# Kernel optimization log

Measured on AMD Instinct MI355X. Metric: run time of the kernel, lower is better.

The kernel has to match this reference:

```python
import jax, jax.numpy as jnp
import numpy as np

N = 100000
E = 800000
IN_NF, IN_EF, OUT_NF, H1, H2 = 64, 16, 64, 32, 32

def _mlp(x, ws, bs):
    last = len(ws) - 1
    for i, (W, b) in enumerate(zip(ws, bs)):
        x = x @ W + b
        if i < last:
            x = jax.nn.leaky_relu(x, 0.2)
    return x

def setup_inputs():
    key = jax.random.key(0)
    ks = iter(jax.random.split(key, 80))
    inp = {}
    inp["nf"] = jax.random.normal(next(ks), (N, IN_NF), jnp.float32)
    inp["ef_out"] = jax.random.normal(next(ks), (E, IN_EF), jnp.float32)
    inp["ef_in"] = jax.random.normal(next(ks), (E, IN_EF), jnp.float32)
    def add_mlp(prefix, sizes):
        for i in range(1, len(sizes)):
            lim = 1.0 / np.sqrt(sizes[i - 1])
            inp[prefix + "_w" + str(i - 1)] = jax.random.uniform(next(ks), (sizes[i - 1], sizes[i]), jnp.float32, -lim, lim)
            inp[prefix + "_b" + str(i - 1)] = jax.random.uniform(next(ks), (sizes[i],), jnp.float32, -lim, lim)
    add_mlp("o2i", (2 * IN_NF + IN_EF, 64, 64, 64, 64, 2 * OUT_NF))
    add_mlp("i2o", (2 * IN_NF + IN_EF, 64, 64, 64, 1 + H1 + H2))
    add_mlp("ri", (IN_NF + 2 * OUT_NF, 64, 64, 64, OUT_NF))
    add_mlp("ro", (IN_NF + H1 + H2, 64, 64, 64, OUT_NF))
    inp["src_out"] = jax.random.randint(next(ks), (E,), 0, N)
    inp["dst_out"] = jax.random.randint(next(ks), (E,), 0, N)
    inp["src_in"] = jax.random.randint(next(ks), (E,), 0, N)
    inp["dst_in"] = jax.random.randint(next(ks), (E,), 0, N)
    idx = jnp.arange(N)
    inp["input_mask"] = idx < (2 * N) // 5
    inp["output_mask"] = idx >= (3 * N) // 5
    return inp

def _forward(nf, ef_out, ef_in, o2i_ws, o2i_bs, i2o_ws, i2o_bs, ri_ws, ri_bs, ro_ws, ro_bs,
             src_out, dst_out, src_in, dst_in, input_mask, output_mask):
    # net_out etype: gather src/dst node feats + edge feats -> MLP -> sum scatter to dst
    xi = jnp.concatenate([nf[src_out], nf[dst_out], ef_out], axis=1)  # [E, 2*in_nf+in_ef]
    efi = _mlp(xi, o2i_ws, o2i_bs)                                    # [E, 2*out_nf]
    nfi = jax.ops.segment_sum(efi, dst_out, num_segments=N)
    new_i = _mlp(jnp.concatenate([nf, nfi], axis=1), ri_ws, ri_bs)    # [N, out_nf]
    # net_in etype: gated edge messages -> mean / max scatter to dst
    xo = jnp.concatenate([nf[src_in], nf[dst_in], ef_in], axis=1)
    m = _mlp(xo, i2o_ws, i2o_bs)                                      # [E, 1+h1+h2]
    k = jax.nn.sigmoid(m[:, :1])
    f1 = m[:, 1:1 + H1] * k
    f2 = m[:, 1 + H1:] * k
    cnt = jax.ops.segment_sum(jnp.ones((E,), nf.dtype), dst_in, num_segments=N)
    nfo1 = jax.ops.segment_sum(f1, dst_in, num_segments=N) / jnp.maximum(cnt, 1.0)[:, None]
    mx = jax.ops.segment_max(f2, dst_in, num_segments=N)
    nfo2 = jnp.where(cnt[:, None] > 0, mx, 0.0)                       # DGL max gives 0 on empty
    new_o = _mlp(jnp.concatenate([nf, nfo1, nfo2], axis=1), ro_ws, ro_bs)
    out = jnp.where(input_mask[:, None], new_i, 0.0)
    out = jnp.where(output_mask[:, None], new_o, out)
    return out

def reference(nf, ef_out, ef_in,
              o2i_w0, o2i_b0, o2i_w1, o2i_b1, o2i_w2, o2i_b2, o2i_w3, o2i_b3, o2i_w4, o2i_b4,
              i2o_w0, i2o_b0, i2o_w1, i2o_b1, i2o_w2, i2o_b2, i2o_w3, i2o_b3,
              ri_w0, ri_b0, ri_w1, ri_b1, ri_w2, ri_b2, ri_w3, ri_b3,
              ro_w0, ro_b0, ro_w1, ro_b1, ro_w2, ro_b2, ro_w3, ro_b3,
              src_out, dst_out, src_in, dst_in, input_mask, output_mask):
    return _forward(nf, ef_out, ef_in,
                    [o2i_w0, o2i_w1, o2i_w2, o2i_w3, o2i_w4], [o2i_b0, o2i_b1, o2i_b2, o2i_b3, o2i_b4],
                    [i2o_w0, i2o_w1, i2o_w2, i2o_w3], [i2o_b0, i2o_b1, i2o_b2, i2o_b3],
                    [ri_w0, ri_w1, ri_w2, ri_w3], [ri_b0, ri_b1, ri_b2, ri_b3],
                    [ro_w0, ro_w1, ro_w2, ro_w3], [ro_b0, ro_b1, ro_b2, ro_b3],
                    src_out, dst_out, src_in, dst_in, input_mask, output_mask)
```

## Files before the change

### kernel.cpp

```cpp
#include <hip/hip_runtime.h>
#include <cmath>

#define THREADS 256

static constexpr int N_NODES   = 100000;
static constexpr int N_EDGES   = 800000;
static constexpr int NIN       = 40000;
static constexpr int NOUT_BASE = 60000;
static constexpr int NOUT      = 40000;
static constexpr int LIST_CAP  = 400000;
static constexpr int CBLK      = 1024;
static constexpr int NBLK      = (N_EDGES + CBLK - 1) / CBLK;

static constexpr size_t OFF_NFI   = 0;
static constexpr size_t OFF_F1    = OFF_NFI   + (size_t)NIN  * 64;
static constexpr size_t OFF_F2    = OFF_F1    + (size_t)NOUT * 32;
static constexpr size_t OFF_CNT   = OFF_F2    + (size_t)NOUT * 32;
static constexpr size_t OFF_CNTO  = OFF_CNT   + NOUT;
static constexpr size_t OFF_CTRO  = OFF_CNTO  + NIN;
static constexpr size_t OFF_CTRI  = OFF_CTRO  + 1;
static constexpr size_t OFF_ZEND  = OFF_CTRI  + 1;
static constexpr size_t OFF_BVEC  = OFF_ZEND;
static constexpr size_t OFF_BCO   = OFF_BVEC + 64;
static constexpr size_t OFF_BCI   = OFF_BCO + NBLK;
static constexpr size_t OFF_LISTO = (OFF_BCI + NBLK + 1) & ~(size_t)1;
static constexpr size_t OFF_LISTI = OFF_LISTO + 2 * (size_t)LIST_CAP;
static constexpr size_t OFF_WB    = (OFF_LISTI + 2 * (size_t)LIST_CAP + 3) & ~(size_t)3;
static constexpr size_t OFF_NFB   = OFF_WB + 47936;

static constexpr unsigned OW_O2I0  = 0;
static constexpr unsigned OW_O2I1  = 10752;
static constexpr unsigned OW_O2I2  = 15360;
static constexpr unsigned OW_O2I3  = 19968;
static constexpr unsigned OW_O2I4C = 24576;
static constexpr unsigned OW_I2O0  = 29184;
static constexpr unsigned OW_I2O1  = 39936;
static constexpr unsigned OW_I2O2  = 44544;
static constexpr unsigned OW_I2O3  = 49152;
static constexpr unsigned OW_RI0   = 54912;
static constexpr unsigned OW_RI1   = 59520;
static constexpr unsigned OW_RI2   = 64128;
static constexpr unsigned OW_RI3   = 68736;
static constexpr unsigned OW_RO0   = 73344;
static constexpr unsigned OW_RO1   = 82048;
static constexpr unsigned OW_RO2   = 86656;
static constexpr unsigned OW_RO3   = 91264;

typedef __attribute__((ext_vector_type(8))) short short8;
typedef __attribute__((ext_vector_type(4))) float f32x4;

__device__ __forceinline__ float lrelu(float x) { return x > 0.0f ? x : 0.2f * x; }

__device__ __forceinline__ unsigned short f2b(float f) {
    unsigned u = __float_as_uint(f);
    return (unsigned short)((u + 0x7fffu + ((u >> 16) & 1u)) >> 16);
}
__device__ __forceinline__ unsigned pk2(float a, float b) {
    return (unsigned)f2b(a) | ((unsigned)f2b(b) << 16);
}
__device__ __forceinline__ short8 cvt8(const float4 va, const float4 vb) {
    union { uint4 u; short8 s; } t;
    t.u = make_uint4(pk2(va.x, va.y), pk2(va.z, va.w), pk2(vb.x, vb.y), pk2(vb.z, vb.w));
    return t.s;
}
__device__ __forceinline__ unsigned fkey(float f) {
    unsigned u = __float_as_uint(f);
    return (u & 0x80000000u) ? ~u : (u | 0x80000000u);
}
__device__ __forceinline__ float funkey(unsigned k) {
    return (k & 0x80000000u) ? __uint_as_float(k & 0x7fffffffu) : __uint_as_float(~k);
}
__device__ __forceinline__ uint2 packm(unsigned s, int d, int e) {
    return make_uint2(s | ((unsigned)(d & 0x7FFF) << 17),
                      (unsigned)e | (((unsigned)d >> 15) << 20));
}

template<int MT, int NT, int KT, int XSTR, int WSTR>
__device__ __forceinline__ void gemm_core(const unsigned short* X, const unsigned short* W,
                                          const float* bias, int biasN, int wv, int lane,
                                          f32x4 (&acc)[MT][NT]) {
    const int r = lane & 15, kg = lane >> 4;
    short8 a[MT][KT];
#pragma unroll
    for (int mt = 0; mt < MT; ++mt)
#pragma unroll
        for (int kk = 0; kk < KT; ++kk)
            a[mt][kk] = *(const short8*)(X + (wv * 16 * MT + mt * 16 + r) * XSTR + kk * 32 + kg * 8);
#pragma unroll
    for (int nt = 0; nt < NT; ++nt) {
        const int c = nt * 16 + r;
        const float bv = (c < biasN) ? bias[c] : 0.0f;
#pragma unroll
        for (int mt = 0; mt < MT; ++mt) acc[mt][nt] = (f32x4){bv, bv, bv, bv};
    }
#pragma unroll
    for (int kk = 0; kk < KT; ++kk)
#pragma unroll
        for (int nt = 0; nt < NT; ++nt) {
            short8 b = *(const short8*)(W + (nt * 16 + r) * WSTR + kk * 32 + kg * 8);
#pragma unroll
            for (int mt = 0; mt < MT; ++mt)
                acc[mt][nt] = __builtin_amdgcn_mfma_f32_16x16x32_bf16(a[mt][kk], b, acc[mt][nt], 0, 0, 0);
        }
}

template<int MT, int NT, int XSTR>
__device__ __forceinline__ void writeback(unsigned short* X, f32x4 (&acc)[MT][NT], int wv, int lane) {
    const int r = lane & 15, kg = lane >> 4;
#pragma unroll
    for (int mt = 0; mt < MT; ++mt)
#pragma unroll
        for (int nt = 0; nt < NT; ++nt)
#pragma unroll
            for (int q = 0; q < 4; ++q)
                X[(wv * 16 * MT + mt * 16 + kg * 4 + q) * XSTR + nt * 16 + r] = f2b(lrelu(acc[mt][nt][q]));
}

template<int NT, int KT, int XSTR, int WSTR>
__device__ __forceinline__ void gemm_w1(const unsigned short* Xw, const unsigned short* W,
                                        const float* bv, int lane, f32x4 (&acc)[NT]) {
    const int r = lane & 15, kg = lane >> 4;
    short8 a[KT];
#pragma unroll
    for (int kk = 0; kk < KT; ++kk)
        a[kk] = *(const short8*)(Xw + r * XSTR + kk * 32 + kg * 8);
#pragma unroll
    for (int nt = 0; nt < NT; ++nt) acc[nt] = (f32x4){bv[nt], bv[nt], bv[nt], bv[nt]};
#pragma unroll
    for (int kk = 0; kk < KT; ++kk)
#pragma unroll
        for (int nt = 0; nt < NT; ++nt) {
            short8 b = *(const short8*)(W + (nt * 16 + r) * WSTR + kk * 32 + kg * 8);
            acc[nt] = __builtin_amdgcn_mfma_f32_16x16x32_bf16(a[kk], b, acc[nt], 0, 0, 0);
        }
}

template<int NT, int XSTR>
__device__ __forceinline__ void writeback_w1(unsigned short* Xw, f32x4 (&acc)[NT], int lane) {
    const int r = lane & 15, kg = lane >> 4;
#pragma unroll
    for (int nt = 0; nt < NT; ++nt)
#pragma unroll
        for (int q = 0; q < 4; ++q)
            Xw[(kg * 4 + q) * XSTR + nt * 16 + r] = f2b(lrelu(acc[nt][q]));
}

struct WDesc { const float* w; int K, N, stride, Np; unsigned off; };
struct WTab { WDesc d[16]; };

__global__ __launch_bounds__(THREADS)
void convert_w(WTab t, unsigned short* wts) {
    const WDesc d = t.d[blockIdx.y];
    const int idx = blockIdx.x * THREADS + threadIdx.x;
    const int tot = d.Np * d.stride;
    if (idx >= tot) return;
    const int n = idx / d.stride, k = idx - n * d.stride;
    const float v = (k < d.K && n < d.N) ? d.w[(size_t)k * d.N + n] : 0.0f;
    wts[d.off + idx] = f2b(v);
}

__global__ __launch_bounds__(THREADS)
void compose_k(const float* __restrict__ w4, const float* __restrict__ rw0,
               const float* __restrict__ b4, unsigned short* __restrict__ wts,
               float* __restrict__ bvec) {
    const int idx = blockIdx.x * THREADS + threadIdx.x;
    if (idx < 4096) {
        const int n = idx >> 6, k = idx & 63;
        float s = 0.0f;
        for (int j = 0; j < 128; ++j) s += w4[k * 128 + j] * rw0[(size_t)(64 + j) * 64 + n];
        wts[OW_O2I4C + n * 72 + k] = f2b(s);
    } else if (idx < 4160) {
        const int n = idx - 4096;
        float s = 0.0f;
        for (int j = 0; j < 128; ++j) s += b4[j] * rw0[(size_t)(64 + j) * 64 + n];
        bvec[n] = s;
    }
}

__global__ __launch_bounds__(THREADS)
void conv_nf_k(const float* __restrict__ nf, unsigned short* __restrict__ nfb) {
    const int i = blockIdx.x * THREADS + threadIdx.x;
    if (i >= N_NODES * 8) return;
    const float4 va = ((const float4*)nf)[i * 2], vb = ((const float4*)nf)[i * 2 + 1];
    *(uint4*)(nfb + (size_t)i * 8) =
        make_uint4(pk2(va.x, va.y), pk2(va.z, va.w), pk2(vb.x, vb.y), pk2(vb.z, vb.w));
}

__global__ __launch_bounds__(THREADS)
void count_k(const int* __restrict__ dst_out, const int* __restrict__ dst_in,
             unsigned* __restrict__ bco, unsigned* __restrict__ bci,
             unsigned* __restrict__ cnt, unsigned* __restrict__ cnto) {
    const int base = blockIdx.x * CBLK;
    const int tid = threadIdx.x, lane = tid & 63, wv = tid >> 6;
    __shared__ unsigned so[4], si[4];
    unsigned co = 0, ci = 0;
#pragma unroll
    for (int it = 0; it < CBLK / THREADS; ++it) {
        const int e = base + it * THREADS + tid;
        bool po = false, pi = false;
        if (e < N_EDGES) {
            const int d0 = dst_out[e];
            if (d0 < NIN) { po = true; atomicAdd(cnto + d0, 1u); }
            const int d1 = dst_in[e];
            if (d1 >= NOUT_BASE) { pi = true; atomicAdd(cnt + (d1 - NOUT_BASE), 1u); }
        }
        const unsigned long long mo = __ballot(po), mi = __ballot(pi);
        if (lane == 0) { co += (unsigned)__popcll(mo); ci += (unsigned)__popcll(mi); }
    }
    if (lane == 0) { so[wv] = co; si[wv] = ci; }
    __syncthreads();
    if (tid == 0) {
        bco[blockIdx.x] = so[0] + so[1] + so[2] + so[3];
        bci[blockIdx.x] = si[0] + si[1] + si[2] + si[3];
    }
}

__global__ __launch_bounds__(128)
void scan_k(unsigned* __restrict__ bco, unsigned* __restrict__ bci,
            unsigned* __restrict__ ctro, unsigned* __restrict__ ctri) {
    const int lane = threadIdx.x & 63;
    unsigned* arr = (threadIdx.x < 64) ? bco : bci;
    unsigned* tot = (threadIdx.x < 64) ? ctro : ctri;
    const int per = (NBLK + 63) / 64;
    const int lo = lane * per;
    const int hi = (lo + per < NBLK) ? lo + per : NBLK;
    unsigned s = 0;
    for (int i = lo; i < hi; ++i) s += arr[i];
    unsigned incl = s;
    for (int d = 1; d < 64; d <<= 1) {
        unsigned v = __shfl_up(incl, d);
        if (lane >= d) incl += v;
    }
    unsigned run = incl - s;
    for (int i = lo; i < hi; ++i) { const unsigned c = arr[i]; arr[i] = run; run += c; }
    if (lane == 63) *tot = incl;
}

__global__ __launch_bounds__(THREADS)
void emit_k(const int* __restrict__ src_out, const int* __restrict__ dst_out,
            const int* __restrict__ src_in, const int* __restrict__ dst_in,
            const unsigned* __restrict__ bco, const unsigned* __restrict__ bci,
            uint2* __restrict__ listo, uint2* __restrict__ listi) {
    const int base = blockIdx.x * CBLK;
    const int tid = threadIdx.x, lane = tid & 63;
    const unsigned long long lm = (1ull << lane) - 1ull;
    __shared__ unsigned lco, lci;
    if (tid == 0) { lco = bco[blockIdx.x]; lci = bci[blockIdx.x]; }
    __syncthreads();
#pragma unroll
    for (int it = 0; it < CBLK / THREADS; ++it) {
        const int e = base + it * THREADS + tid;
        bool po = false, pi = false;
        int d0 = 0, d1 = 0;
        if (e < N_EDGES) {
            d0 = dst_out[e]; po = d0 < NIN;
            d1 = dst_in[e];  pi = d1 >= NOUT_BASE;
        }
        const unsigned long long mo = __ballot(po), mi = __ballot(pi);
        unsigned b0v = 0, b1v = 0;
        if (lane == 0) {
            if (mo) b0v = atomicAdd(&lco, (unsigned)__popcll(mo));
            if (mi) b1v = atomicAdd(&lci, (unsigned)__popcll(mi));
        }
        b0v = (unsigned)__shfl((int)b0v, 0);
        b1v = (unsigned)__shfl((int)b1v, 0);
        if (po) listo[b0v + (unsigned)__popcll(mo & lm)] = packm((unsigned)src_out[e], d0, e);
        if (pi) listi[b1v + (unsigned)__popcll(mi & lm)] = packm((unsigned)src_in[e], d1, e);
    }
}

__device__ __forceinline__ void gather_a(short8 (&a)[5], const unsigned short* nfb, const float* ef,
                                         int e16, int s16, int d16, int kg) {
    const short8 z = {0, 0, 0, 0, 0, 0, 0, 0};
    if (e16 >= 0) {
        const unsigned short* ps = nfb + (size_t)s16 * 64 + kg * 8;
        const unsigned short* pd = nfb + (size_t)d16 * 64 + kg * 8;
        a[0] = *(const short8*)ps;
        a[1] = *(const short8*)(ps + 32);
        a[2] = *(const short8*)pd;
        a[3] = *(const short8*)(pd + 32);
        if (kg < 2) {
            const float* pe = ef + (size_t)e16 * 16 + kg * 8;
            a[4] = cvt8(((const float4*)pe)[0], ((const float4*)pe)[1]);
        } else a[4] = z;
    } else { a[0] = z; a[1] = z; a[2] = z; a[3] = z; a[4] = z; }
}

__global__ __launch_bounds__(512, 4)
void edge_out_mfma(const unsigned short* __restrict__ nfb, const float* __restrict__ ef,
                   const uint2* __restrict__ list, const unsigned* __restrict__ counter,
                   const unsigned short* __restrict__ wts,
                   const float* __restrict__ b0, const float* __restrict__ b1,
                   const float* __restrict__ b2, const float* __restrict__ b3,
                   float* __restrict__ nfi) {
    __shared__ unsigned short W[24576];
    __shared__ unsigned short X[128 * 72];
    const int tid = threadIdx.x, lane = tid & 63, wv = tid >> 6;
    const int r = lane & 15, kg = lane >> 4;
    for (int i = tid * 8; i < 24576; i += 512 * 8)
        *(uint4*)(W + i) = *(const uint4*)(wts + OW_O2I0 + i);
    float bv0[4], bv1[4], bv2[4], bv3[4];
    const float bz[4] = {0.0f, 0.0f, 0.0f, 0.0f};
#pragma unroll
    for (int nt = 0; nt < 4; ++nt) {
        bv0[nt] = b0[nt * 16 + r]; bv1[nt] = b1[nt * 16 + r];
        bv2[nt] = b2[nt * 16 + r]; bv3[nt] = b3[nt * 16 + r];
    }
    unsigned short* Xw = X + wv * 16 * 72;
    const unsigned short* W4C = wts + OW_O2I4C;
    const unsigned total = *counter;
    const unsigned nchunks = (total + 15) >> 4;
    __syncthreads();

    for (unsigned c = blockIdx.x * 8 + wv; c < nchunks; c += (unsigned)gridDim.x * 8) {
        const unsigned ebase = c << 4;
        int my_e = -1, my_s = 0, my_d = -1;
        if (lane < 16 && ebase + (unsigned)lane < total) {
            const uint2 m = list[ebase + lane];
            my_s = (int)(m.x & 0x1FFFFu);
            my_d = (int)(((m.x >> 17) & 0x7FFFu) | (((m.y >> 20) & 3u) << 15));
            my_e = (int)(m.y & 0xFFFFFu);
        }
        const int e16 = __shfl(my_e, r), s16 = __shfl(my_s, r), d16 = __shfl(my_d, r);
        short8 a[5];
        gather_a(a, nfb, ef, e16, s16, d16, kg);
        f32x4 acc[4];
#pragma unroll
        for (int nt = 0; nt < 4; ++nt) acc[nt] = (f32x4){bv0[nt], bv0[nt], bv0[nt], bv0[nt]};
#pragma unroll
        for (int kk = 0; kk < 5; ++kk)
#pragma unroll
            for (int nt = 0; nt < 4; ++nt) {
                short8 b = *(const short8*)(W + (nt * 16 + r) * 168 + kk * 32 + kg * 8);
                acc[nt] = __builtin_amdgcn_mfma_f32_16x16x32_bf16(a[kk], b, acc[nt], 0, 0, 0);
            }
        writeback_w1<4, 72>(Xw, acc, lane);
        gemm_w1<4, 2, 72, 72>(Xw, W + 10752, bv1, lane, acc); writeback_w1<4, 72>(Xw, acc, lane);
        gemm_w1<4, 2, 72, 72>(Xw, W + 15360, bv2, lane, acc); writeback_w1<4, 72>(Xw, acc, lane);
        gemm_w1<4, 2, 72, 72>(Xw, W + 19968, bv3, lane, acc); writeback_w1<4, 72>(Xw, acc, lane);
        f32x4 acc4[4];
        gemm_w1<4, 2, 72, 72>(Xw, W4C, bz, lane, acc4);
        int re[4], rd[4];
#pragma unroll
        for (int q = 0; q < 4; ++q) {
            re[q] = __shfl(my_e, kg * 4 + q);
            rd[q] = __shfl(my_d, kg * 4 + q);
        }
        float s[4];
        int cur = -1;
#pragma unroll
        for (int q = 0; q < 4; ++q) {
            if (re[q] < 0) break;
            if (rd[q] != cur) {
                if (cur >= 0) {
                    float* p = nfi + (size_t)cur * 64;
#pragma unroll
                    for (int nt = 0; nt < 4; ++nt) atomicAdd(p + nt * 16 + r, s[nt]);
                }
                cur = rd[q];
#pragma unroll
                for (int nt = 0; nt < 4; ++nt) s[nt] = acc4[nt][q];
            } else {
#pragma unroll
                for (int nt = 0; nt < 4; ++nt) s[nt] += acc4[nt][q];
            }
        }
        if (cur >= 0) {
            float* p = nfi + (size_t)cur * 64;
#pragma unroll
            for (int nt = 0; nt < 4; ++nt) atomicAdd(p + nt * 16 + r, s[nt]);
        }
    }
}

__global__ __launch_bounds__(512, 4)
void edge_in_mfma(const unsigned short* __restrict__ nfb, const float* __restrict__ ef,
                  const uint2* __restrict__ list, const unsigned* __restrict__ counter,
                  const unsigned short* __restrict__ wts,
                  const float* __restrict__ b0, const float* __restrict__ b1,
                  const float* __restrict__ b2, const float* __restrict__ b3,
                  float* __restrict__ f1s, unsigned* __restrict__ f2k) {
    __shared__ unsigned short W[25728];
    __shared__ unsigned short X[128 * 72];
    const int tid = threadIdx.x, lane = tid & 63, wv = tid >> 6;
    const int r = lane & 15, kg = lane >> 4;
    for (int i = tid * 8; i < 25728; i += 512 * 8)
        *(uint4*)(W + i) = *(const uint4*)(wts + OW_I2O0 + i);
    float bv0[4], bv1[4], bv2[4], bv3[5];
#pragma unroll
    for (int nt = 0; nt < 4; ++nt) {
        bv0[nt] = b0[nt * 16 + r]; bv1[nt] = b1[nt * 16 + r]; bv2[nt] = b2[nt * 16 + r];
        bv3[nt] = b3[nt * 16 + r];
    }
    bv3[4] = (r == 0) ? b3[64] : 0.0f;
    unsigned short* Xw = X + wv * 16 * 72;
    const unsigned total = *counter;
    const unsigned nchunks = (total + 15) >> 4;
    bool valid[5], isadd[5];
#pragma unroll
    for (int nt = 0; nt < 5; ++nt) {
        const int cc = nt * 16 + r;
        valid[nt] = (cc >= 1 && cc <= 64);
        isadd[nt] = (cc <= 32);
    }
    __syncthreads();

    for (unsigned c = blockIdx.x * 8 + wv; c < nchunks; c += (unsigned)gridDim.x * 8) {
        const unsigned ebase = c << 4;
        int my_e = -1, my_s = 0, my_d = -1;
        if (lane < 16 && ebase + (unsigned)lane < total) {
            const uint2 m = list[ebase + lane];
            my_s = (int)(m.x & 0x1FFFFu);
            my_d = (int)(((m.x >> 17) & 0x7FFFu) | (((m.y >> 20) & 3u) << 15));
            my_e = (int)(m.y & 0xFFFFFu);
        }
        const int e16 = __shfl(my_e, r), s16 = __shfl(my_s, r), d16 = __shfl(my_d, r);
        short8 a[5];
        gather_a(a, nfb, ef, e16, s16, d16, kg);
        f32x4 acc[4];
#pragma unroll
        for (int nt = 0; nt < 4; ++nt) acc[nt] = (f32x4){bv0[nt], bv0[nt], bv0[nt], bv0[nt]};
#pragma unroll
        for (int kk = 0; kk < 5; ++kk)
#pragma unroll
            for (int nt = 0; nt < 4; ++nt) {
                short8 b = *(const short8*)(W + (nt * 16 + r) * 168 + kk * 32 + kg * 8);
                acc[nt] = __builtin_amdgcn_mfma_f32_16x16x32_bf16(a[kk], b, acc[nt], 0, 0, 0);
            }
        writeback_w1<4, 72>(Xw, acc, lane);
        gemm_w1<4, 2, 72, 72>(Xw, W + 10752, bv1, lane, acc); writeback_w1<4, 72>(Xw, acc, lane);
        gemm_w1<4, 2, 72, 72>(Xw, W + 15360, bv2, lane, acc); writeback_w1<4, 72>(Xw, acc, lane);
        f32x4 acc5[5];
        gemm_w1<5, 2, 72, 72>(Xw, W + 19968, bv3, lane, acc5);
        int re[4], rd[4];
        float rgv[4];
#pragma unroll
        for (int q = 0; q < 4; ++q) {
            re[q]  = __shfl(my_e, kg * 4 + q);
            rd[q]  = __shfl(my_d, kg * 4 + q);
            rgv[q] = __shfl(acc5[4][q], lane & 48);
        }
        float s[5];
        int cur = -1;
        auto flush = [&](int d) {
            if (d < 0) return;
            const int rr = d - NOUT_BASE;
            if (valid[0]) atomicAdd(f1s + (size_t)rr * 32 + (r - 1), s[0]);
            if (valid[1]) atomicAdd(f1s + (size_t)rr * 32 + 15 + r, s[1]);
            if (valid[2]) {
                if (isadd[2]) atomicAdd(f1s + (size_t)rr * 32 + 31, s[2]);
                else          atomicMax(f2k + (size_t)rr * 32 + (r - 1), fkey(s[2]));
            }
            if (valid[3]) atomicMax(f2k + (size_t)rr * 32 + 15 + r, fkey(s[3]));
            if (valid[4]) atomicMax(f2k + (size_t)rr * 32 + 31, fkey(s[4]));
        };
#pragma unroll
        for (int q = 0; q < 4; ++q) {
            if (re[q] < 0) break;
            const float kgv = 1.0f / (1.0f + expf(-rgv[q]));
            if (rd[q] != cur) {
                flush(cur);
                cur = rd[q];
#pragma unroll
                for (int nt = 0; nt < 5; ++nt) s[nt] = acc5[nt][q] * kgv;
            } else {
#pragma unroll
                for (int nt = 0; nt < 5; ++nt) {
                    const float v = acc5[nt][q] * kgv;
                    s[nt] = isadd[nt] ? s[nt] + v : fmaxf(s[nt], v);
                }
            }
        }
        flush(cur);
    }
}

__global__ __launch_bounds__(THREADS)
void node_ri_mfma(const unsigned short* __restrict__ nfb, const float* __restrict__ nfi,
                  const unsigned* __restrict__ cnto, const float* __restrict__ bvec,
                  const unsigned short* __restrict__ wts,
                  const float* __restrict__ b0, const float* __restrict__ b1,
                  const float* __restrict__ b2, const float* __restrict__ b3,
                  float* __restrict__ out) {
    __shared__ unsigned short X[64 * 72];
    __shared__ unsigned short Wl[4608];
    const int tid = threadIdx.x, lane = tid & 63, wv = tid >> 6;
    const int base = blockIdx.x * 64;
    for (int i = tid; i < 64 * 8; i += THREADS) {
        const int el = i >> 3, q = i & 7;
        *(uint4*)(X + el * 72 + q * 8) = *(const uint4*)(nfb + (size_t)(base + el) * 64 + q * 8);
    }
    auto stage = [&](unsigned off) {
        for (int i = tid * 8; i < 4608; i += THREADS * 8)
            *(uint4*)(Wl + i) = *(const uint4*)(wts + off + i);
    };
    stage(OW_RI0);
    __syncthreads();
    const int r = lane & 15, kg = lane >> 4;
    f32x4 acc[1][4];
    gemm_core<1, 4, 2, 72, 72>(X, Wl, b0, 64, wv, lane, acc);
    {
        float bvv[4];
#pragma unroll
        for (int nt = 0; nt < 4; ++nt) bvv[nt] = bvec[nt * 16 + r];
#pragma unroll
        for (int q = 0; q < 4; ++q) {
            const int node = base + wv * 16 + kg * 4 + q;
            const float cf = (float)cnto[node];
#pragma unroll
            for (int nt = 0; nt < 4; ++nt)
                acc[0][nt][q] += nfi[(size_t)node * 64 + nt * 16 + r] + cf * bvv[nt];
        }
    }
    writeback<1, 4, 72>(X, acc, wv, lane);
    __syncthreads(); stage(OW_RI1); __syncthreads();
    gemm_core<1, 4, 2, 72, 72>(X, Wl, b1, 64, wv, lane, acc);
    writeback<1, 4, 72>(X, acc, wv, lane);
    __syncthreads(); stage(OW_RI2); __syncthreads();
    gemm_core<1, 4, 2, 72, 72>(X, Wl, b2, 64, wv, lane, acc);
    writeback<1, 4, 72>(X, acc, wv, lane);
    __syncthreads(); stage(OW_RI3); __syncthreads();
    gemm_core<1, 4, 2, 72, 72>(X, Wl, b3, 64, wv, lane, acc);
#pragma unroll
    for (int nt = 0; nt < 4; ++nt)
#pragma unroll
        for (int q = 0; q < 4; ++q)
            out[(size_t)(base + wv * 16 + kg * 4 + q) * 64 + nt * 16 + r] = acc[0][nt][q];
}

__global__ __launch_bounds__(THREADS)
void node_ro_mfma(const float* __restrict__ nf, const float* __restrict__ f1s,
                  const unsigned* __restrict__ f2k, const unsigned* __restrict__ cnt,
                  const unsigned short* __restrict__ wts,
                  const float* __restrict__ b0, const float* __restrict__ b1,
                  const float* __restrict__ b2, const float* __restrict__ b3,
                  float* __restrict__ out) {
    __shared__ unsigned short X[64 * 136];
    __shared__ unsigned short Wl[8704];
    const int tid = threadIdx.x, lane = tid & 63, wv = tid >> 6;
    const int rbase = blockIdx.x * 64;
    for (int i = tid; i < 64 * 17; i += THREADS) {
        const int el = i / 17, q = i - el * 17;
        const int rr = rbase + el;
        unsigned p0 = 0, p1 = 0, p2 = 0, p3 = 0;
        if (q < 16) {
            float v[8];
            if (q < 8) {
                const float* sp = nf + (size_t)(NOUT_BASE + rr) * 64 + q * 8;
                const float4 va = *(const float4*)sp, vb = *(const float4*)(sp + 4);
                v[0]=va.x; v[1]=va.y; v[2]=va.z; v[3]=va.w; v[4]=vb.x; v[5]=vb.y; v[6]=vb.z; v[7]=vb.w;
            } else {
                const unsigned cc = cnt[rr];
                if (q < 12) {
                    const float inv = 1.0f / fmaxf((float)cc, 1.0f);
#pragma unroll
                    for (int j = 0; j < 8; ++j) v[j] = f1s[(size_t)rr * 32 + (q - 8) * 8 + j] * inv;
                } else {
#pragma unroll
                    for (int j = 0; j < 8; ++j)
                        v[j] = (cc > 0u) ? funkey(f2k[(size_t)rr * 32 + (q - 12) * 8 + j]) : 0.0f;
                }
            }
            p0 = pk2(v[0], v[1]); p1 = pk2(v[2], v[3]); p2 = pk2(v[4], v[5]); p3 = pk2(v[6], v[7]);
        }
        *(uint4*)(X + el * 136 + q * 8) = make_uint4(p0, p1, p2, p3);
    }
    auto stage = [&](unsigned off, int n) {
        for (int i = tid * 8; i < n; i += THREADS * 8)
            *(uint4*)(Wl + i) = *(const uint4*)(wts + off + i);
    };
    stage(OW_RO0, 8704);
    __syncthreads();
    f32x4 acc[1][4];
    gemm_core<1, 4, 4, 136, 136>(X, Wl, b0, 64, wv, lane, acc);
    writeback<1, 4, 136>(X, acc, wv, lane);
    __syncthreads(); stage(OW_RO1, 4608); __syncthreads();
    gemm_core<1, 4, 2, 136, 72>(X, Wl, b1, 64, wv, lane, acc);
    writeback<1, 4, 136>(X, acc, wv, lane);
    __syncthreads(); stage(OW_RO2, 4608); __syncthreads();
    gemm_core<1, 4, 2, 136, 72>(X, Wl, b2, 64, wv, lane, acc);
    writeback<1, 4, 136>(X, acc, wv, lane);
    __syncthreads(); stage(OW_RO3, 4608); __syncthreads();
    gemm_core<1, 4, 2, 136, 72>(X, Wl, b3, 64, wv, lane, acc);
    const int r = lane & 15, kg = lane >> 4;
#pragma unroll
    for (int nt = 0; nt < 4; ++nt)
#pragma unroll
        for (int q = 0; q < 4; ++q)
            out[(size_t)(NOUT_BASE + rbase + wv * 16 + kg * 4 + q) * 64 + nt * 16 + r] = acc[0][nt][q];
}

extern "C" void kernel_launch(void* const* d_in, const int* in_sizes, int n_in,
                              void* d_out, int out_size, void* d_ws, size_t ws_size,
                              hipStream_t stream) {
    const float* nf     = (const float*)d_in[0];
    const float* ef_out = (const float*)d_in[1];
    const float* ef_in  = (const float*)d_in[2];
    const float* o2i_w[5] = {(const float*)d_in[3], (const float*)d_in[5], (const float*)d_in[7], (const float*)d_in[9], (const float*)d_in[11]};
    const float* o2i_b[5] = {(const float*)d_in[4], (const float*)d_in[6], (const float*)d_in[8], (const float*)d_in[10], (const float*)d_in[12]};
    const float* i2o_w[4] = {(const float*)d_in[13], (const float*)d_in[15], (const float*)d_in[17], (const float*)d_in[19]};
    const float* i2o_b[4] = {(const float*)d_in[14], (const float*)d_in[16], (const float*)d_in[18], (const float*)d_in[20]};
    const float* ri_w[4]  = {(const float*)d_in[21], (const float*)d_in[23], (const float*)d_in[25], (const float*)d_in[27]};
    const float* ri_b[4]  = {(const float*)d_in[22], (const float*)d_in[24], (const float*)d_in[26], (const float*)d_in[28]};
    const float* ro_w[4]  = {(const float*)d_in[29], (const float*)d_in[31], (const float*)d_in[33], (const float*)d_in[35]};
    const float* ro_b[4]  = {(const float*)d_in[30], (const float*)d_in[32], (const float*)d_in[34], (const float*)d_in[36]};
    const int* src_out  = (const int*)d_in[37];
    const int* dst_out  = (const int*)d_in[38];
    const int* src_in   = (const int*)d_in[39];
    const int* dst_in   = (const int*)d_in[40];

    unsigned* ws    = (unsigned*)d_ws;
    float*    nfi   = (float*)(ws + OFF_NFI);
    float*    f1s   = (float*)(ws + OFF_F1);
    unsigned* f2k   = ws + OFF_F2;
    unsigned* cnt   = ws + OFF_CNT;
    unsigned* cnto  = ws + OFF_CNTO;
    unsigned* ctro  = ws + OFF_CTRO;
    unsigned* ctri  = ws + OFF_CTRI;
    float*    bvec  = (float*)(ws + OFF_BVEC);
    unsigned* bco   = ws + OFF_BCO;
    unsigned* bci   = ws + OFF_BCI;
    uint2*    lsto  = (uint2*)(ws + OFF_LISTO);
    uint2*    lsti  = (uint2*)(ws + OFF_LISTI);
    unsigned short* wts = (unsigned short*)(ws + OFF_WB);
    unsigned short* nfb = (unsigned short*)(ws + OFF_NFB);

    hipMemsetAsync(d_ws, 0, OFF_ZEND * sizeof(unsigned), stream);
    hipMemsetAsync((char*)d_out + (size_t)NIN * 64 * sizeof(float), 0,
                   (size_t)(NOUT_BASE - NIN) * 64 * sizeof(float), stream);

    WTab t;
    t.d[0]  = {o2i_w[0], 144,  64, 168,  64, OW_O2I0};
    t.d[1]  = {o2i_w[1],  64,  64,  72,  64, OW_O2I1};
    t.d[2]  = {o2i_w[2],  64,  64,  72,  64, OW_O2I2};
    t.d[3]  = {o2i_w[3],  64,  64,  72,  64, OW_O2I3};
    t.d[4]  = {i2o_w[0], 144,  64, 168,  64, OW_I2O0};
    t.d[5]  = {i2o_w[1],  64,  64,  72,  64, OW_I2O1};
    t.d[6]  = {i2o_w[2],  64,  64,  72,  64, OW_I2O2};
    t.d[7]  = {i2o_w[3],  64,  65,  72,  80, OW_I2O3};
    t.d[8]  = {ri_w[0],   64,  64,  72,  64, OW_RI0};
    t.d[9]  = {ri_w[1],   64,  64,  72,  64, OW_RI1};
    t.d[10] = {ri_w[2],   64,  64,  72,  64, OW_RI2};
    t.d[11] = {ri_w[3],   64,  64,  72,  64, OW_RI3};
    t.d[12] = {ro_w[0],  128,  64, 136,  64, OW_RO0};
    t.d[13] = {ro_w[1],   64,  64,  72,  64, OW_RO1};
    t.d[14] = {ro_w[2],   64,  64,  72,  64, OW_RO2};
    t.d[15] = {ro_w[3],   64,  64,  72,  64, OW_RO3};
    convert_w<<<dim3(50, 16), THREADS, 0, stream>>>(t, wts);
    compose_k<<<17, THREADS, 0, stream>>>(o2i_w[4], ri_w[0], o2i_b[4], wts, bvec);
    conv_nf_k<<<(N_NODES * 8 + THREADS - 1) / THREADS, THREADS, 0, stream>>>(nf, nfb);

    count_k<<<NBLK, THREADS, 0, stream>>>(dst_out, dst_in, bco, bci, cnt, cnto);
    scan_k<<<1, 128, 0, stream>>>(bco, bci, ctro, ctri);
    emit_k<<<NBLK, THREADS, 0, stream>>>(src_out, dst_out, src_in, dst_in, bco, bci, lsto, lsti);

    edge_out_mfma<<<512, 512, 0, stream>>>(
        nfb, ef_out, lsto, ctro, wts,
        o2i_b[0], o2i_b[1], o2i_b[2], o2i_b[3], nfi);

    edge_in_mfma<<<512, 512, 0, stream>>>(
        nfb, ef_in, lsti, ctri, wts,
        i2o_b[0], i2o_b[1], i2o_b[2], i2o_b[3], f1s, f2k);

    node_ri_mfma<<<NIN / 64, THREADS, 0, stream>>>(
        nfb, nfi, cnto, bvec, wts, ri_b[0], ri_b[1], ri_b[2], ri_b[3], (float*)d_out);

    node_ro_mfma<<<NOUT / 64, THREADS, 0, stream>>>(
        nf, f1s, f2k, cnt, wts, ro_b[0], ro_b[1], ro_b[2], ro_b[3], (float*)d_out);
}
```

Measured before the change: 323.9 us.

## Replace compacted edge lists with destination-sorted counting-sort buckets

Swaps block-level stream compaction of filtered edges for a full counting sort by destination node. A histogram kernel is followed by a two-block exclusive scan over per-node counts, and emit then scatters each edge to its node's slot through per-node atomics. Edges sharing a destination end up contiguous, which is meant to improve locality and cut atomic contention in the downstream segment-sum, mean and max reductions inside the edge MFMA kernels. The cost is a scan over 40k nodes done by a single block per list and scattered atomic writes in emit. The ctr counters and bvec move out of the zeroed region, and ctr now comes from the scan.

```diff
diff --git a/kernel.cpp b/kernel.cpp
--- a/kernel.cpp
+++ b/kernel.cpp
@@ -9,21 +9,19 @@
 static constexpr int NOUT_BASE = 60000;
 static constexpr int NOUT      = 40000;
 static constexpr int LIST_CAP  = 400000;
-static constexpr int CBLK      = 1024;
-static constexpr int NBLK      = (N_EDGES + CBLK - 1) / CBLK;
 
 static constexpr size_t OFF_NFI   = 0;
 static constexpr size_t OFF_F1    = OFF_NFI   + (size_t)NIN  * 64;
 static constexpr size_t OFF_F2    = OFF_F1    + (size_t)NOUT * 32;
 static constexpr size_t OFF_CNT   = OFF_F2    + (size_t)NOUT * 32;
 static constexpr size_t OFF_CNTO  = OFF_CNT   + NOUT;
-static constexpr size_t OFF_CTRO  = OFF_CNTO  + NIN;
+static constexpr size_t OFF_ZEND  = OFF_CNTO  + NIN;
+static constexpr size_t OFF_CTRO  = OFF_ZEND;
 static constexpr size_t OFF_CTRI  = OFF_CTRO  + 1;
-static constexpr size_t OFF_ZEND  = OFF_CTRI  + 1;
-static constexpr size_t OFF_BVEC  = OFF_ZEND;
-static constexpr size_t OFF_BCO   = OFF_BVEC + 64;
-static constexpr size_t OFF_BCI   = OFF_BCO + NBLK;
-static constexpr size_t OFF_LISTO = (OFF_BCI + NBLK + 1) & ~(size_t)1;
+static constexpr size_t OFF_BVEC  = OFF_CTRI  + 1;
+static constexpr size_t OFF_OFFSO = OFF_BVEC + 64;
+static constexpr size_t OFF_OFFSI = OFF_OFFSO + NIN;
+static constexpr size_t OFF_LISTO = (OFF_OFFSI + NOUT + 1) & ~(size_t)1;
 static constexpr size_t OFF_LISTI = OFF_LISTO + 2 * (size_t)LIST_CAP;
 static constexpr size_t OFF_WB    = (OFF_LISTI + 2 * (size_t)LIST_CAP + 3) & ~(size_t)3;
 static constexpr size_t OFF_NFB   = OFF_WB + 47936;
@@ -187,85 +185,58 @@
 }
 
 __global__ __launch_bounds__(THREADS)
-void count_k(const int* __restrict__ dst_out, const int* __restrict__ dst_in,
-             unsigned* __restrict__ bco, unsigned* __restrict__ bci,
-             unsigned* __restrict__ cnt, unsigned* __restrict__ cnto) {
-    const int base = blockIdx.x * CBLK;
+void hist_k(const int* __restrict__ dst_out, const int* __restrict__ dst_in,
+            unsigned* __restrict__ cnto, unsigned* __restrict__ cnt) {
+    const int e = blockIdx.x * THREADS + threadIdx.x;
+    const int d0 = dst_out[e];
+    if (d0 < NIN) atomicAdd(cnto + d0, 1u);
+    const int d1 = dst_in[e];
+    if (d1 >= NOUT_BASE) atomicAdd(cnt + (d1 - NOUT_BASE), 1u);
+}
+
+__global__ __launch_bounds__(1024)
+void scan2_k(const unsigned* __restrict__ cnto, const unsigned* __restrict__ cnt,
+             unsigned* __restrict__ offso, unsigned* __restrict__ offsi,
+             unsigned* __restrict__ ctro, unsigned* __restrict__ ctri) {
+    const unsigned* h = (blockIdx.x == 0) ? cnto : cnt;
+    unsigned* o       = (blockIdx.x == 0) ? offso : offsi;
+    unsigned* tot     = (blockIdx.x == 0) ? ctro : ctri;
     const int tid = threadIdx.x, lane = tid & 63, wv = tid >> 6;
-    __shared__ unsigned so[4], si[4];
-    unsigned co = 0, ci = 0;
-#pragma unroll
-    for (int it = 0; it < CBLK / THREADS; ++it) {
-        const int e = base + it * THREADS + tid;
-        bool po = false, pi = false;
-        if (e < N_EDGES) {
-            const int d0 = dst_out[e];
-            if (d0 < NIN) { po = true; atomicAdd(cnto + d0, 1u); }
-            const int d1 = dst_in[e];
-            if (d1 >= NOUT_BASE) { pi = true; atomicAdd(cnt + (d1 - NOUT_BASE), 1u); }
-        }
-        const unsigned long long mo = __ballot(po), mi = __ballot(pi);
-        if (lane == 0) { co += (unsigned)__popcll(mo); ci += (unsigned)__popcll(mi); }
-    }
-    if (lane == 0) { so[wv] = co; si[wv] = ci; }
+    const int lo = tid * 40;
+    const int hi = (lo + 40 < NIN) ? lo + 40 : NIN;
+    unsigned s = 0;
+    for (int i = lo; i < hi; ++i) s += h[i];
+    unsigned incl = s;
+    for (int d = 1; d < 64; d <<= 1) { unsigned v = __shfl_up(incl, d); if (lane >= d) incl += v; }
+    __shared__ unsigned wsum[16], woff[16];
+    if (lane == 63) wsum[wv] = incl;
     __syncthreads();
-    if (tid == 0) {
-        bco[blockIdx.x] = so[0] + so[1] + so[2] + so[3];
-        bci[blockIdx.x] = si[0] + si[1] + si[2] + si[3];
-    }
-}
-
-__global__ __launch_bounds__(128)
-void scan_k(unsigned* __restrict__ bco, unsigned* __restrict__ bci,
-            unsigned* __restrict__ ctro, unsigned* __restrict__ ctri) {
-    const int lane = threadIdx.x & 63;
-    unsigned* arr = (threadIdx.x < 64) ? bco : bci;
-    unsigned* tot = (threadIdx.x < 64) ? ctro : ctri;
-    const int per = (NBLK + 63) / 64;
-    const int lo = lane * per;
-    const int hi = (lo + per < NBLK) ? lo + per : NBLK;
-    unsigned s = 0;
-    for (int i = lo; i < hi; ++i) s += arr[i];
-    unsigned incl = s;
-    for (int d = 1; d < 64; d <<= 1) {
-        unsigned v = __shfl_up(incl, d);
-        if (lane >= d) incl += v;
-    }
-    unsigned run = incl - s;
-    for (int i = lo; i < hi; ++i) { const unsigned c = arr[i]; arr[i] = run; run += c; }
-    if (lane == 63) *tot = incl;
+    if (tid < 16) {
+        unsigned v = wsum[tid], sc = v;
+        for (int d = 1; d < 16; d <<= 1) { unsigned t2 = __shfl_up(sc, d); if (tid >= d) sc += t2; }
+        woff[tid] = sc - v;
+    }
+    __syncthreads();
+    unsigned run = woff[wv] + incl - s;
+    for (int i = lo; i < hi; ++i) { const unsigned c = h[i]; o[i] = run; run += c; }
+    if (hi == NIN && lo < NIN) *tot = run;
 }
 
 __global__ __launch_bounds__(THREADS)
 void emit_k(const int* __restrict__ src_out, const int* __restrict__ dst_out,
             const int* __restrict__ src_in, const int* __restrict__ dst_in,
-            const unsigned* __restrict__ bco, const unsigned* __restrict__ bci,
+            unsigned* __restrict__ offso, unsigned* __restrict__ offsi,
             uint2* __restrict__ listo, uint2* __restrict__ listi) {
-    const int base = blockIdx.x * CBLK;
-    const int tid = threadIdx.x, lane = tid & 63;
-    const unsigned long long lm = (1ull << lane) - 1ull;
-    __shared__ unsigned lco, lci;
-    if (tid == 0) { lco = bco[blockIdx.x]; lci = bci[blockIdx.x]; }
-    __syncthreads();
-#pragma unroll
-    for (int it = 0; it < CBLK / THREADS; ++it) {
-        const int e = base + it * THREADS + tid;
-        bool po = false, pi = false;
-        int d0 = 0, d1 = 0;
-        if (e < N_EDGES) {
-            d0 = dst_out[e]; po = d0 < NIN;
-            d1 = dst_in[e];  pi = d1 >= NOUT_BASE;
-        }
-        const unsigned long long mo = __ballot(po), mi = __ballot(pi);
-        unsigned b0v = 0, b1v = 0;
-        if (lane == 0) {
-            if (mo) b0v = atomicAdd(&lco, (unsigned)__popcll(mo));
-            if (mi) b1v = atomicAdd(&lci, (unsigned)__popcll(mi));
-        }
-        b0v = (unsigned)__shfl((int)b0v, 0);
-        b1v = (unsigned)__shfl((int)b1v, 0);
-        if (po) listo[b0v + (unsigned)__popcll(mo & lm)] = packm((unsigned)src_out[e], d0, e);
-        if (pi) listi[b1v + (unsigned)__popcll(mi & lm)] = packm((unsigned)src_in[e], d1, e);
+    const int e = blockIdx.x * THREADS + threadIdx.x;
+    const int d0 = dst_out[e];
+    if (d0 < NIN) {
+        const unsigned p = atomicAdd(offso + d0, 1u);
+        if (p < (unsigned)LIST_CAP) listo[p] = packm((unsigned)src_out[e], d0, e);
+    }
+    const int d1 = dst_in[e];
+    if (d1 >= NOUT_BASE) {
+        const unsigned p = atomicAdd(offsi + (d1 - NOUT_BASE), 1u);
+        if (p < (unsigned)LIST_CAP) listi[p] = packm((unsigned)src_in[e], d1, e);
     }
 }
 
@@ -618,8 +589,8 @@
     unsigned* ctro  = ws + OFF_CTRO;
     unsigned* ctri  = ws + OFF_CTRI;
     float*    bvec  = (float*)(ws + OFF_BVEC);
-    unsigned* bco   = ws + OFF_BCO;
-    unsigned* bci   = ws + OFF_BCI;
+    unsigned* offso = ws + OFF_OFFSO;
+    unsigned* offsi = ws + OFF_OFFSI;
     uint2*    lsto  = (uint2*)(ws + OFF_LISTO);
     uint2*    lsti  = (uint2*)(ws + OFF_LISTI);
     unsigned short* wts = (unsigned short*)(ws + OFF_WB);
@@ -650,9 +621,10 @@
     compose_k<<<17, THREADS, 0, stream>>>(o2i_w[4], ri_w[0], o2i_b[4], wts, bvec);
     conv_nf_k<<<(N_NODES * 8 + THREADS - 1) / THREADS, THREADS, 0, stream>>>(nf, nfb);
 
-    count_k<<<NBLK, THREADS, 0, stream>>>(dst_out, dst_in, bco, bci, cnt, cnto);
-    scan_k<<<1, 128, 0, stream>>>(bco, bci, ctro, ctri);
-    emit_k<<<NBLK, THREADS, 0, stream>>>(src_out, dst_out, src_in, dst_in, bco, bci, lsto, lsti);
+    hist_k<<<N_EDGES / THREADS, THREADS, 0, stream>>>(dst_out, dst_in, cnto, cnt);
+    scan2_k<<<2, 1024, 0, stream>>>(cnto, cnt, offso, offsi, ctro, ctri);
+    emit_k<<<N_EDGES / THREADS, THREADS, 0, stream>>>(
+        src_out, dst_out, src_in, dst_in, offso, offsi, lsto, lsti);
 
     edge_out_mfma<<<512, 512, 0, stream>>>(
         nfb, ef_out, lsto, ctro, wts,
```

New measurement: 358.2 us. 1.11x slower.
